# Performance work log

Measured on AMD Instinct MI355X. Metric: run time of the kernel, lower is better.

The kernel has to match this reference:

```python
import jax, jax.numpy as jnp
import numpy as np

N_QUBITS = 4
N_LAYERS = 3
LETTERS = "ijkl"  # one axis label per qubit; batch axis is 'b'
CNOT = np.array([[1, 0, 0, 0], [0, 1, 0, 0], [0, 0, 0, 1], [0, 0, 1, 0]], dtype=np.complex64).reshape(2, 2, 2, 2)


def _apply_1q(state, U, w, batched):
    # state: [B,2,2,2,2]; U: [2,2] (shared) or [B,2,2] (per-sample)
    s = "b" + LETTERS
    t = LETTERS[w]
    u = ("b" if batched else "") + "z" + t
    return jnp.einsum(f"{u},{s}->{s.replace(t, 'z')}", U, state)


def _apply_cnot(state, c, t):
    s = "b" + LETTERS
    a, b = LETTERS[c], LETTERS[t]
    out = s.replace(a, "x").replace(b, "y")
    return jnp.einsum(f"xy{a}{b},{s}->{out}", jnp.asarray(CNOT), state)


def _rx(theta):
    # theta: [B] -> batched RX gates [B,2,2]
    c = jnp.cos(theta / 2).astype(jnp.complex64)
    s = (-1j * jnp.sin(theta / 2)).astype(jnp.complex64)
    return jnp.stack([jnp.stack([c, s], -1), jnp.stack([s, c], -1)], -2)


def _rz(a):
    e = jnp.exp(-1j * a.astype(jnp.complex64) / 2)
    zero = jnp.zeros((), jnp.complex64)
    return jnp.array([[e, zero], [zero, jnp.conj(e)]])


def _ry(a):
    c = jnp.cos(a / 2).astype(jnp.complex64)
    s = jnp.sin(a / 2).astype(jnp.complex64)
    return jnp.array([[c, -s], [s, c]])


def _rot(phi, theta, omega):
    # PennyLane Rot = RZ(omega) @ RY(theta) @ RZ(phi)
    return _rz(omega) @ _ry(theta) @ _rz(phi)


def _circuit(qparams, z):
    # qparams: [n_layers, n_qubits, 3] float32; z: [B, n_qubits] float32
    B = z.shape[0]
    state = jnp.zeros((B,) + (2,) * N_QUBITS, jnp.complex64)
    state = state.at[:, 0, 0, 0, 0].set(1.0 + 0.0j)
    # data-encoding RX layer (per-sample angles -> batched gates)
    for w in range(N_QUBITS):
        state = _apply_1q(state, _rx(z[:, w]), w, batched=True)
    # variational layers: Rot on every wire then CNOT ladder
    for layer in range(N_LAYERS):
        for w in range(N_QUBITS):
            U = _rot(qparams[layer, w, 0], qparams[layer, w, 1], qparams[layer, w, 2])
            state = _apply_1q(state, U, w, batched=False)
        for w in range(N_QUBITS - 1):
            state = _apply_cnot(state, w, w + 1)
    probs = jnp.abs(state) ** 2  # [B,2,2,2,2] float32
    zsign = jnp.array([1.0, -1.0], jnp.float32)
    s = "b" + LETTERS
    evs = [jnp.einsum(f"{s},{LETTERS[w]}->b", probs, zsign) for w in range(N_QUBITS)]
    return jnp.stack(evs, axis=-1)  # [B, n_qubits]


def reference(x, enc_w, enc_b, qparams, cls_w, cls_b, bn_gamma, bn_beta):
    B = x.shape[0]
    # avg_pool2d(kernel_size=6) on 28x28 -> 4x4 (floor division drops last 4 rows/cols)
    pooled = x[:, :, :24, :24].reshape(B, 1, 4, 6, 4, 6).mean(axis=(3, 5)).reshape(B, 16)
    z = pooled @ enc_w.T + enc_b  # [B, n_qubits]
    evs = _circuit(qparams, z)    # [B, n_qubits]
    out = evs @ cls_w.T + cls_b   # [B, output_dim]
    # BatchNorm1d in training mode: biased batch statistics, eps=1e-5
    mu = out.mean(axis=0)
    var = ((out - mu) ** 2).mean(axis=0)
    out = (out - mu) / jnp.sqrt(var + 1e-5) * bn_gamma + bn_beta
    return out


def setup_inputs() -> dict:
    key = jax.random.key(0)
    ks = jax.random.split(key, 6)
    B = 32768
    return {
        "x": jax.random.normal(ks[0], (B, 1, 28, 28), jnp.float32),
        "enc_w": jax.random.normal(ks[1], (N_QUBITS, 16), jnp.float32) * 0.25,
        "enc_b": jnp.zeros((N_QUBITS,), jnp.float32),
        "qparams": jax.random.normal(ks[2], (N_LAYERS, N_QUBITS, 3), jnp.float32),
        "cls_w": jax.random.normal(ks[3], (4, N_QUBITS), jnp.float32) * 0.5,
        "cls_b": jnp.zeros((4,), jnp.float32),
        "bn_gamma": jnp.ones((4,), jnp.float32),
        "bn_beta": jnp.zeros((4,), jnp.float32),
    }
```

## Files before the change

### kernel.cpp

```cpp
#include <hip/hip_runtime.h>
#include <math.h>


#define BTOT 32768
#define SPB  16
#define NBLK (BTOT / SPB)
#define SSTR 576

__device__ float g_prep[576];
__device__ float g_pooled[BTOT * 16];
__device__ float g_partials[NBLK * 8];

__global__ __launch_bounds__(64) void prep_kernel(
    const float* __restrict__ qparams, const float* __restrict__ cls_w)
{
    const int t = threadIdx.x;
    {
        int j = t >> 4, i = t & 15;
        float acc = 0.f;
        #pragma unroll
        for (int w = 0; w < 4; ++w)
            acc += cls_w[j * 4 + w] * ((i & (8 >> w)) ? -1.f : 1.f);
        g_prep[512 + j * 16 + i] = acc;
    }
    if (t < 16) {
        float pr[16], pi[16];
        #pragma unroll
        for (int i = 0; i < 16; ++i) { pr[i] = (i == t) ? 1.f : 0.f; pi[i] = 0.f; }
        #pragma unroll
        for (int layer = 0; layer < 3; ++layer) {
            #pragma unroll
            for (int w = 0; w < 4; ++w) {
                const float* qp = qparams + (layer * 4 + w) * 3;
                float phi = qp[0], th = qp[1], om = qp[2];
                float c, s, ca, sa, cd, sd;
                __sincosf(0.5f * th, &s, &c);
                __sincosf(0.5f * (phi + om), &sa, &ca);
                __sincosf(0.5f * (phi - om), &sd, &cd);
                float u00r =  c * ca, u00i = -c * sa;
                float u01r = -s * cd, u01i = -s * sd;
                float u10r =  s * cd, u10i = -s * sd;
                float u11r =  c * ca, u11i =  c * sa;
                const int m = 8 >> w;
                #pragma unroll
                for (int idx = 0; idx < 16; ++idx) {
                    if (idx & m) continue;
                    const int i1 = idx | m;
                    float ar = pr[idx], ai = pi[idx], br = pr[i1], bi = pi[i1];
                    pr[idx] = u00r*ar - u00i*ai + u01r*br - u01i*bi;
                    pi[idx] = u00r*ai + u00i*ar + u01r*bi + u01i*br;
                    pr[i1]  = u10r*ar - u10i*ai + u11r*br - u11i*bi;
                    pi[i1]  = u10r*ai + u10i*ar + u11r*bi + u11i*br;
                }
            }
            #pragma unroll
            for (int w = 0; w < 3; ++w) {
                const int mc = 8 >> w, mt = 8 >> (w + 1);
                #pragma unroll
                for (int idx = 0; idx < 16; ++idx) {
                    if ((idx & mc) && !(idx & mt)) {
                        const int i1 = idx | mt;
                        float tr = pr[idx], ti = pi[idx];
                        pr[idx] = pr[i1]; pi[idx] = pi[i1];
                        pr[i1] = tr;      pi[i1] = ti;
                    }
                }
            }
        }
        const int p = __popc(t) & 3;
        #pragma unroll
        for (int i = 0; i < 16; ++i) {
            float re = pr[i], im = pi[i], vr, vi;
            if (p == 0)      { vr = re;  vi = im;  }
            else if (p == 1) { vr = im;  vi = -re; }
            else if (p == 2) { vr = -re; vi = -im; }
            else             { vr = -im; vi = re;  }
            g_prep[i * 16 + t]       = vr;
            g_prep[256 + i * 16 + t] = vi;
        }
    }
}

__global__ __launch_bounds__(256) void pool_kernel(const float* __restrict__ x)
{
    __shared__ __align__(16) float sx[SPB * SSTR];

    const int tid = threadIdx.x;
    const int s0  = blockIdx.x * SPB;
    const float4* xb = (const float4*)x;

    float4 st[9];
    #pragma unroll
    for (int it = 0; it < 9; ++it) {
        const int gid  = it * 256 + tid;
        const int c    = gid / 144;
        const int o    = gid - c * 144;
        const int row  = o / 6;
        const int col4 = o - row * 6;
        st[it] = xb[(size_t)(s0 + c) * 196 + row * 7 + col4];
    }
    #pragma unroll
    for (int it = 0; it < 9; ++it)
        ((float4*)sx)[it * 256 + tid] = st[it];

    __syncthreads();

    const int s = tid >> 4, cell = tid & 15;
    const int cr = cell >> 2, cc = cell & 3;
    int srot = s;
    srot -= (srot >= 12) ? 12 : ((srot >= 6) ? 6 : 0);
    const float* sb = &sx[s * SSTR + cr * 6 * 24 + cc * 6];
    float sum = 0.f;
    #pragma unroll
    for (int rr = 0; rr < 6; ++rr) {
        int r = rr + srot; r -= (r >= 6) ? 6 : 0;
        const float2* rp = (const float2*)(sb + r * 24);
        float2 a = rp[0], b = rp[1], c2 = rp[2];
        sum += (a.x + a.y) + (b.x + b.y) + (c2.x + c2.y);
    }
    g_pooled[(size_t)(s0 + s) * 16 + cell] = sum * (1.f / 36.f);
}

__global__ __launch_bounds__(256) void qc_kernel(
    const float* __restrict__ enc_w, const float* __restrict__ enc_b,
    const float* __restrict__ cls_b,
    float* __restrict__ preBN)
{
    __shared__ float sVr[16 * 17];
    __shared__ float sVi[16 * 17];
    __shared__ float sW2[4 * 17];
    __shared__ float red[4][8];

    const int tid = threadIdx.x;
    const int s0  = blockIdx.x * SPB;
    const int s = tid >> 4, cell = tid & 15;

    const float pv = g_pooled[(size_t)(s0 + s) * 16 + cell];

    #pragma unroll
    for (int g0 = 0; g0 < 576; g0 += 256) {
        int g = g0 + tid;
        if (g < 576) {
            float v = g_prep[g];
            int row = (g >> 4) & 15, col = g & 15;
            if (g < 256)      sVr[row * 17 + col] = v;
            else if (g < 512) sVi[row * 17 + col] = v;
            else              sW2[(g - 512) / 16 * 17 + col] = v;
        }
    }

    float z[4];
    #pragma unroll
    for (int j = 0; j < 4; ++j) z[j] = enc_w[j * 16 + cell] * pv;
    #pragma unroll
    for (int m = 1; m <= 8; m <<= 1) {
        #pragma unroll
        for (int j = 0; j < 4; ++j) z[j] += __shfl_xor(z[j], m, 64);
    }
    #pragma unroll
    for (int j = 0; j < 4; ++j) z[j] += enc_b[j];

    float cz[4], sz[4];
    #pragma unroll
    for (int j = 0; j < 4; ++j) __sincosf(0.5f * z[j], &sz[j], &cz[j]);
    float a01[4] = {cz[0]*cz[1], cz[0]*sz[1], sz[0]*cz[1], sz[0]*sz[1]};
    float a23[4] = {cz[2]*cz[3], cz[2]*sz[3], sz[2]*cz[3], sz[2]*sz[3]};
    float rv[16];
    #pragma unroll
    for (int k = 0; k < 16; ++k) rv[k] = a01[k >> 2] * a23[k & 3];

    __syncthreads();

    float ar = 0.f, ai = 0.f;
    #pragma unroll
    for (int k = 0; k < 16; ++k) {
        ar += sVr[cell * 17 + k] * rv[k];
        ai += sVi[cell * 17 + k] * rv[k];
    }
    const float prob = ar * ar + ai * ai;
    float out[4];
    #pragma unroll
    for (int j = 0; j < 4; ++j) out[j] = sW2[j * 17 + cell] * prob;
    #pragma unroll
    for (int m = 1; m <= 8; m <<= 1) {
        #pragma unroll
        for (int j = 0; j < 4; ++j) out[j] += __shfl_xor(out[j], m, 64);
    }
    #pragma unroll
    for (int j = 0; j < 4; ++j) out[j] += cls_b[j];

    if (cell == 0)
        ((float4*)preBN)[s0 + s] = make_float4(out[0], out[1], out[2], out[3]);

    const float w = (cell == 0) ? 1.f : 0.f;
    float v8[8] = {out[0]*w, out[1]*w, out[2]*w, out[3]*w,
                   out[0]*out[0]*w, out[1]*out[1]*w, out[2]*out[2]*w, out[3]*out[3]*w};
    #pragma unroll
    for (int m = 0; m < 8; ++m) {
        v8[m] += __shfl_down(v8[m], 32, 64);
        v8[m] += __shfl_down(v8[m], 16, 64);
    }
    const int wave = tid >> 6, lane = tid & 63;
    if (lane == 0) {
        #pragma unroll
        for (int m = 0; m < 8; ++m) red[wave][m] = v8[m];
    }
    __syncthreads();
    if (tid < 8)
        g_partials[blockIdx.x * 8 + tid] =
            red[0][tid] + red[1][tid] + red[2][tid] + red[3][tid];
}

__global__ __launch_bounds__(256) void bn_kernel(
    const float* __restrict__ gamma, const float* __restrict__ beta,
    float* __restrict__ out)
{
    const int tid = threadIdx.x;
    float acc[8] = {0, 0, 0, 0, 0, 0, 0, 0};
    const float4* p4 = (const float4*)g_partials;
    #pragma unroll
    for (int it = 0; it < NBLK / 256; ++it) {
        int b = it * 256 + tid;
        float4 a = p4[b * 2], c = p4[b * 2 + 1];
        acc[0] += a.x; acc[1] += a.y; acc[2] += a.z; acc[3] += a.w;
        acc[4] += c.x; acc[5] += c.y; acc[6] += c.z; acc[7] += c.w;
    }
    #pragma unroll
    for (int off = 32; off >= 1; off >>= 1) {
        #pragma unroll
        for (int m = 0; m < 8; ++m) acc[m] += __shfl_xor(acc[m], off, 64);
    }
    __shared__ float red[4][8];
    const int wave = tid >> 6, lane = tid & 63;
    if (lane == 0) {
        #pragma unroll
        for (int m = 0; m < 8; ++m) red[wave][m] = acc[m];
    }
    __syncthreads();
    float sums[8];
    #pragma unroll
    for (int m = 0; m < 8; ++m)
        sums[m] = red[0][m] + red[1][m] + red[2][m] + red[3][m];

    const int s = blockIdx.x * 256 + tid;
    const float invB = 1.f / (float)BTOT;
    float4 v = ((const float4*)out)[s];
    float o[4] = {v.x, v.y, v.z, v.w};
    #pragma unroll
    for (int j = 0; j < 4; ++j) {
        float mu   = sums[j] * invB;
        float var  = sums[4 + j] * invB - mu * mu;
        float rstd = rsqrtf(var + 1e-5f);
        o[j] = (o[j] - mu) * rstd * gamma[j] + beta[j];
    }
    ((float4*)out)[s] = make_float4(o[0], o[1], o[2], o[3]);
}

extern "C" void kernel_launch(void* const* d_in, const int* in_sizes, int n_in,
                              void* d_out, int out_size, void* d_ws, size_t ws_size,
                              hipStream_t stream)
{
    const float* x        = (const float*)d_in[0];
    const float* enc_w    = (const float*)d_in[1];
    const float* enc_b    = (const float*)d_in[2];
    const float* qparams  = (const float*)d_in[3];
    const float* cls_w    = (const float*)d_in[4];
    const float* cls_b    = (const float*)d_in[5];
    const float* bn_gamma = (const float*)d_in[6];
    const float* bn_beta  = (const float*)d_in[7];

    float* outp = (float*)d_out;
    (void)d_ws; (void)ws_size;

    prep_kernel<<<1, 64, 0, stream>>>(qparams, cls_w);
    pool_kernel<<<NBLK, 256, 0, stream>>>(x);
    qc_kernel<<<NBLK, 256, 0, stream>>>(enc_w, enc_b, cls_b, outp);
    bn_kernel<<<128, 256, 0, stream>>>(bn_gamma, bn_beta, outp);
}
```

Measured before the change: 179.0 us.

## Fuse pooling into quantum-circuit kernel with one wave per sample

```diff
diff --git a/kernel.cpp b/kernel.cpp
--- a/kernel.cpp
+++ b/kernel.cpp
@@ -3,13 +3,11 @@
 
 
 #define BTOT 32768
-#define SPB  16
-#define NBLK (BTOT / SPB)
-#define SSTR 576
+#define WPB  4
+#define NBLK2 (BTOT / WPB)
 
 __device__ float g_prep[576];
-__device__ float g_pooled[BTOT * 16];
-__device__ float g_partials[NBLK * 8];
+__device__ float g_partials[NBLK2 * 8];
 
 __global__ __launch_bounds__(64) void prep_kernel(
     const float* __restrict__ qparams, const float* __restrict__ cls_w)
@@ -81,47 +79,8 @@
     }
 }
 
-__global__ __launch_bounds__(256) void pool_kernel(const float* __restrict__ x)
-{
-    __shared__ __align__(16) float sx[SPB * SSTR];
-
-    const int tid = threadIdx.x;
-    const int s0  = blockIdx.x * SPB;
-    const float4* xb = (const float4*)x;
-
-    float4 st[9];
-    #pragma unroll
-    for (int it = 0; it < 9; ++it) {
-        const int gid  = it * 256 + tid;
-        const int c    = gid / 144;
-        const int o    = gid - c * 144;
-        const int row  = o / 6;
-        const int col4 = o - row * 6;
-        st[it] = xb[(size_t)(s0 + c) * 196 + row * 7 + col4];
-    }
-    #pragma unroll
-    for (int it = 0; it < 9; ++it)
-        ((float4*)sx)[it * 256 + tid] = st[it];
-
-    __syncthreads();
-
-    const int s = tid >> 4, cell = tid & 15;
-    const int cr = cell >> 2, cc = cell & 3;
-    int srot = s;
-    srot -= (srot >= 12) ? 12 : ((srot >= 6) ? 6 : 0);
-    const float* sb = &sx[s * SSTR + cr * 6 * 24 + cc * 6];
-    float sum = 0.f;
-    #pragma unroll
-    for (int rr = 0; rr < 6; ++rr) {
-        int r = rr + srot; r -= (r >= 6) ? 6 : 0;
-        const float2* rp = (const float2*)(sb + r * 24);
-        float2 a = rp[0], b = rp[1], c2 = rp[2];
-        sum += (a.x + a.y) + (b.x + b.y) + (c2.x + c2.y);
-    }
-    g_pooled[(size_t)(s0 + s) * 16 + cell] = sum * (1.f / 36.f);
-}
-
-__global__ __launch_bounds__(256) void qc_kernel(
+__global__ __launch_bounds__(256) void qfc_kernel(
+    const float* __restrict__ x,
     const float* __restrict__ enc_w, const float* __restrict__ enc_b,
     const float* __restrict__ cls_b,
     float* __restrict__ preBN)
@@ -129,13 +88,19 @@
     __shared__ float sVr[16 * 17];
     __shared__ float sVi[16 * 17];
     __shared__ float sW2[4 * 17];
-    __shared__ float red[4][8];
+    __shared__ float sEw[64];
+    __shared__ float red[WPB][8];
 
     const int tid = threadIdx.x;
-    const int s0  = blockIdx.x * SPB;
-    const int s = tid >> 4, cell = tid & 15;
-
-    const float pv = g_pooled[(size_t)(s0 + s) * 16 + cell];
+    const int l   = tid & 63, wid = tid >> 6;
+    const int smp = blockIdx.x * WPB + wid;
+
+    const float4* base4 = (const float4*)(x + (size_t)smp * 784);
+    const int o0 = l, o1 = l + 64, o2 = l + 128;
+    float4 v0 = base4[(o0 / 6) * 7 + (o0 % 6)];
+    float4 v1 = base4[(o1 / 6) * 7 + (o1 % 6)];
+    float4 v2 = make_float4(0.f, 0.f, 0.f, 0.f);
+    if (l < 16) v2 = base4[(o2 / 6) * 7 + (o2 % 6)];
 
     #pragma unroll
     for (int g0 = 0; g0 < 576; g0 += 256) {
@@ -148,17 +113,37 @@
             else              sW2[(g - 512) / 16 * 17 + col] = v;
         }
     }
-
+    if (tid < 64) sEw[tid] = enc_w[tid];
+    __syncthreads();
+
+    float pz[4] = {0.f, 0.f, 0.f, 0.f};
+    auto FOLD = [&](int o, float4 v) {
+        const int c4 = o % 6;
+        const int r  = o / 6;
+        const int rb = r / 6;
+        const float lo = v.x + v.y, hi = v.z + v.w;
+        const int ca = (4 * c4) / 6;
+        const bool split = (c4 == 1) | (c4 == 4);
+        const float sA = split ? lo : (lo + hi);
+        #pragma unroll
+        for (int j = 0; j < 4; ++j) {
+            float w = sEw[j * 16 + rb * 4 + ca] * sA;
+            if (split) w += sEw[j * 16 + rb * 4 + ca + 1] * hi;
+            pz[j] += w;
+        }
+    };
+    FOLD(o0, v0);
+    FOLD(o1, v1);
+    if (l < 16) FOLD(o2, v2);
+
+    #pragma unroll
+    for (int m = 1; m <= 32; m <<= 1) {
+        #pragma unroll
+        for (int j = 0; j < 4; ++j) pz[j] += __shfl_xor(pz[j], m, 64);
+    }
     float z[4];
     #pragma unroll
-    for (int j = 0; j < 4; ++j) z[j] = enc_w[j * 16 + cell] * pv;
-    #pragma unroll
-    for (int m = 1; m <= 8; m <<= 1) {
-        #pragma unroll
-        for (int j = 0; j < 4; ++j) z[j] += __shfl_xor(z[j], m, 64);
-    }
-    #pragma unroll
-    for (int j = 0; j < 4; ++j) z[j] += enc_b[j];
+    for (int j = 0; j < 4; ++j) z[j] = pz[j] * (1.f / 36.f) + enc_b[j];
 
     float cz[4], sz[4];
     #pragma unroll
@@ -169,18 +154,17 @@
     #pragma unroll
     for (int k = 0; k < 16; ++k) rv[k] = a01[k >> 2] * a23[k & 3];
 
-    __syncthreads();
-
+    const int i = l & 15;
     float ar = 0.f, ai = 0.f;
     #pragma unroll
     for (int k = 0; k < 16; ++k) {
-        ar += sVr[cell * 17 + k] * rv[k];
-        ai += sVi[cell * 17 + k] * rv[k];
+        ar += sVr[i * 17 + k] * rv[k];
+        ai += sVi[i * 17 + k] * rv[k];
     }
     const float prob = ar * ar + ai * ai;
     float out[4];
     #pragma unroll
-    for (int j = 0; j < 4; ++j) out[j] = sW2[j * 17 + cell] * prob;
+    for (int j = 0; j < 4; ++j) out[j] = sW2[j * 17 + i] * prob;
     #pragma unroll
     for (int m = 1; m <= 8; m <<= 1) {
         #pragma unroll
@@ -189,26 +173,21 @@
     #pragma unroll
     for (int j = 0; j < 4; ++j) out[j] += cls_b[j];
 
-    if (cell == 0)
-        ((float4*)preBN)[s0 + s] = make_float4(out[0], out[1], out[2], out[3]);
-
-    const float w = (cell == 0) ? 1.f : 0.f;
-    float v8[8] = {out[0]*w, out[1]*w, out[2]*w, out[3]*w,
-                   out[0]*out[0]*w, out[1]*out[1]*w, out[2]*out[2]*w, out[3]*out[3]*w};
-    #pragma unroll
-    for (int m = 0; m < 8; ++m) {
-        v8[m] += __shfl_down(v8[m], 32, 64);
-        v8[m] += __shfl_down(v8[m], 16, 64);
-    }
-    const int wave = tid >> 6, lane = tid & 63;
-    if (lane == 0) {
-        #pragma unroll
-        for (int m = 0; m < 8; ++m) red[wave][m] = v8[m];
+    if (l == 0) {
+        ((float4*)preBN)[smp] = make_float4(out[0], out[1], out[2], out[3]);
+        #pragma unroll
+        for (int j = 0; j < 4; ++j) {
+            red[wid][j]     = out[j];
+            red[wid][4 + j] = out[j] * out[j];
+        }
     }
     __syncthreads();
-    if (tid < 8)
-        g_partials[blockIdx.x * 8 + tid] =
-            red[0][tid] + red[1][tid] + red[2][tid] + red[3][tid];
+    if (tid < 8) {
+        float a = 0.f;
+        #pragma unroll
+        for (int w = 0; w < WPB; ++w) a += red[w][tid];
+        g_partials[blockIdx.x * 8 + tid] = a;
+    }
 }
 
 __global__ __launch_bounds__(256) void bn_kernel(
@@ -219,7 +198,7 @@
     float acc[8] = {0, 0, 0, 0, 0, 0, 0, 0};
     const float4* p4 = (const float4*)g_partials;
     #pragma unroll
-    for (int it = 0; it < NBLK / 256; ++it) {
+    for (int it = 0; it < NBLK2 / 256; ++it) {
         int b = it * 256 + tid;
         float4 a = p4[b * 2], c = p4[b * 2 + 1];
         acc[0] += a.x; acc[1] += a.y; acc[2] += a.z; acc[3] += a.w;
@@ -273,7 +252,6 @@
     (void)d_ws; (void)ws_size;
 
     prep_kernel<<<1, 64, 0, stream>>>(qparams, cls_w);
-    pool_kernel<<<NBLK, 256, 0, stream>>>(x);
-    qc_kernel<<<NBLK, 256, 0, stream>>>(enc_w, enc_b, cls_b, outp);
+    qfc_kernel<<<NBLK2, 256, 0, stream>>>(x, enc_w, enc_b, cls_b, outp);
     bn_kernel<<<128, 256, 0, stream>>>(bn_gamma, bn_beta, outp);
 }
```

Measured after the change: 179.7 us. About the same (+0.4%).
